# Kernel optimization log

Hardware: AMD Instinct MI355X
Metric: run time of the kernel (lower is better)

The kernel has to match this reference:

```python
import jax, jax.numpy as jnp
import numpy as np

N_NODES = 50000
N_EDGES = 800000
N_FEAT = 128
N_HID = 128
N_LAYER = 4
N_CLASS = 40


def setup_inputs() -> dict:
    key = jax.random.key(0)
    ks = jax.random.split(key, 8)
    x = jax.random.normal(ks[0], (N_NODES, N_FEAT), jnp.float32)
    edge_index = jax.random.randint(ks[1], (2, N_EDGES), 0, N_NODES, dtype=jnp.int64)
    s = 1.0 / np.float32(np.sqrt(N_HID))
    # n_feat == n_hid so all L conv weights stack into one [L, C, C] tensor
    convW = jax.random.normal(ks[2], (N_LAYER, N_HID, N_HID), jnp.float32) * s
    convb = jnp.zeros((N_LAYER, N_HID), jnp.float32)
    W_att = jax.random.normal(ks[3], (N_HID, N_HID), jnp.float32) * s
    a_att = jax.random.normal(ks[4], (N_HID,), jnp.float32) * s
    W_out = jax.random.normal(ks[5], (N_HID, N_CLASS), jnp.float32) * s
    b_out = jnp.zeros((N_CLASS,), jnp.float32)
    return dict(x=x, edge_index=edge_index, convW=convW, convb=convb,
                W_att=W_att, a_att=a_att, W_out=W_out, b_out=b_out)


def reference(x, edge_index, convW, convb, W_att, a_att, W_out, b_out):
    src, dst = edge_index[0], edge_index[1]
    N = x.shape[0]
    # GCN symmetric normalization with self-loops: deg = 1 + in-degree
    deg = jax.ops.segment_sum(jnp.ones_like(dst, dtype=jnp.float32), dst,
                              num_segments=N) + 1.0
    dinv = jax.lax.rsqrt(deg)
    enorm = (dinv[src] * dinv[dst])[:, None]   # per-edge norm
    snorm = (dinv * dinv)[:, None]             # self-loop norm

    hs = []
    h = x
    for l in range(N_LAYER):
        hW = h @ convW[l]                                          # [N, C]
        agg = jax.ops.segment_sum(hW[src] * enorm, dst, num_segments=N)
        agg = agg + hW * snorm                                     # self-loop
        h = jax.nn.relu(agg + convb[l])
        # dropout is identity at inference (training=False)
        hs.append(h)

    H = jnp.stack(hs, axis=1)                                      # [N, L, C]
    # additive attention over layers: alpha_l = softmax_l(a . tanh(W h_l))
    scores = jnp.tanh(H @ W_att) @ a_att                           # [N, L]
    alpha = jax.nn.softmax(scores, axis=1)
    fused = jnp.einsum('nl,nlc->nc', alpha, H)                     # [N, C]
    return fused @ W_out + b_out                                   # [N, n_class]
```

## Files before the change

kernel.cpp:

```cpp
#include <hip/hip_runtime.h>

#define NNODES 50000
#define NEDGES 800000
#define NCLASS 40
#define GEMMB 782
#define XBLK  3125
#define WELL  64

#define EBLK  782
#define PREPB 80
#define WOUTB 6
#define BSHIFT 10
#define NB    49
#define BUCKCAP 20480

typedef _Float16 half8  __attribute__((ext_vector_type(8)));
typedef float    floatx4 __attribute__((ext_vector_type(4)));

#define CSTR 136
#define SMEM_BYTES (64 * CSTR * 2 + 256)

__device__ __forceinline__ float fast_tanh(float x) {
    return 1.0f - 2.0f / (__expf(2.0f * x) + 1.0f);
}

__global__ __launch_bounds__(1024) void k_part(const int* __restrict__ src, const int* __restrict__ dst,
                                               int* __restrict__ gbase, int2* __restrict__ ebuf,
                                               const float* __restrict__ convW, const float* __restrict__ W_att,
                                               _Float16* __restrict__ WT,
                                               const float* __restrict__ Wout, _Float16* __restrict__ WoutT) {
    int bid = blockIdx.x, tid = threadIdx.x;
    if (bid < EBLK) {
        __shared__ int hist[NB];
        __shared__ int base[NB];
        if (tid < NB) hist[tid] = 0;
        __syncthreads();
        int e = bid * 1024 + tid;
        bool ok = e < NEDGES;
        int s = 0, d = 0, b = 0, slot = 0;
        if (ok) {
            d = dst[e];
            s = src[e];
            b = d >> BSHIFT;
            slot = atomicAdd(&hist[b], 1);
        }
        __syncthreads();
        if (tid < NB) base[tid] = atomicAdd(&gbase[tid * 32], hist[tid]);
        __syncthreads();
        if (ok) {
            int pos = base[b] + slot;
            if (pos < BUCKCAP) ebuf[(size_t)b * BUCKCAP + pos] = make_int2(s, d);
        }
    } else if (bid < EBLK + PREPB) {
        int idx = (bid - EBLK) * 1024 + tid;
        int mat = idx >> 14, rem = idx & 16383;
        int j = rem & 7, lane = (rem >> 3) & 63, tile = rem >> 9;
        int l15 = lane & 15, quad = lane >> 4;
        int ct = tile & 7, kk = tile >> 3;
        int n = ct * 16 + l15, k = kk * 32 + quad * 8 + j;
        const float* s = (mat < 4) ? (convW + mat * 16384) : W_att;
        WT[idx] = (_Float16)s[k * 128 + n];
    } else {
        int idx = (bid - EBLK - PREPB) * 1024 + tid;
        int j = idx & 7, lane = (idx >> 3) & 63, tile = idx >> 9;
        int l15 = lane & 15, quad = lane >> 4;
        int ct = tile % 3, kk = tile / 3;
        int n = ct * 16 + l15, k = kk * 32 + quad * 8 + j;
        WoutT[idx] = (n < NCLASS) ? (_Float16)Wout[k * NCLASS + n] : (_Float16)0.f;
    }
}

__global__ __launch_bounds__(1024) void k_build(const int* __restrict__ gbase, const int2* __restrict__ ebuf,
                                                int* __restrict__ esrc, int* __restrict__ cnt) {
    __shared__ int lcnt[1024];
    int b = blockIdx.x, t = threadIdx.x;
    lcnt[t] = 0;
    __syncthreads();
    int n0 = b << BSHIFT;
    int total = gbase[b * 32];
    if (total > BUCKCAP) total = BUCKCAP;
    const int2* ep = ebuf + (size_t)b * BUCKCAP;
    for (int i = t; i < total; i += 1024) {
        int2 p = ep[i];
        int slot = atomicAdd(&lcnt[p.y - n0], 1);
        if (slot < WELL) esrc[p.y * WELL + slot] = p.x;
    }
    __syncthreads();
    int n = n0 + t;
    if (n < NNODES) cnt[n] = (lcnt[t] < WELL) ? lcnt[t] : WELL;
}

__global__ __launch_bounds__(256) void k_gemm0(const float* __restrict__ Av, const _Float16* __restrict__ WTf,
                                               const int* __restrict__ cnt, _Float16* __restrict__ C) {
    __shared__ __align__(16) char smem[SMEM_BYTES];
    _Float16 (*Csh)[CSTR] = (_Float16 (*)[CSTR])smem;
    float* sdinv = (float*)(smem + 64 * CSTR * 2);
    int m0 = blockIdx.x * 64;
    int tid = threadIdx.x;
    int wave = tid >> 6, lane = tid & 63;
    int quad = lane >> 4, l15 = lane & 15;
    int ko = quad * 8;

    if (tid < 64) {
        int r = m0 + tid; if (r > NNODES - 1) r = NNODES - 1;
        sdinv[tid] = rsqrtf((float)cnt[r] + 1.0f);
    }

    floatx4 acc[4][2];
#pragma unroll
    for (int rt = 0; rt < 4; ++rt)
#pragma unroll
        for (int ct = 0; ct < 2; ++ct) acc[rt][ct] = (floatx4){0.f, 0.f, 0.f, 0.f};

#pragma unroll
    for (int kk = 0; kk < 4; ++kk) {
        half8 a[4], b[2];
#pragma unroll
        for (int rt = 0; rt < 4; ++rt) {
            int row = m0 + rt * 16 + l15;
            if (row > NNODES - 1) row = NNODES - 1;
            const float* Ap = Av + (size_t)row * 128 + kk * 32 + ko;
            float4 f0 = *(const float4*)Ap;
            float4 f1 = *(const float4*)(Ap + 4);
            a[rt] = (half8){(_Float16)f0.x, (_Float16)f0.y, (_Float16)f0.z, (_Float16)f0.w,
                            (_Float16)f1.x, (_Float16)f1.y, (_Float16)f1.z, (_Float16)f1.w};
        }
#pragma unroll
        for (int ct = 0; ct < 2; ++ct)
            b[ct] = *(const half8*)&WTf[((kk * 8 + (wave * 2 + ct)) * 64 + lane) * 8];
#pragma unroll
        for (int rt = 0; rt < 4; ++rt)
#pragma unroll
            for (int ct = 0; ct < 2; ++ct)
                acc[rt][ct] = __builtin_amdgcn_mfma_f32_16x16x32_f16(a[rt], b[ct], acc[rt][ct], 0, 0, 0);
    }
    __syncthreads();

#pragma unroll
    for (int rt = 0; rt < 4; ++rt)
#pragma unroll
        for (int r = 0; r < 4; ++r) {
            float d = sdinv[rt * 16 + quad * 4 + r];
#pragma unroll
            for (int ct = 0; ct < 2; ++ct)
                Csh[rt * 16 + quad * 4 + r][wave * 32 + ct * 16 + l15] = (_Float16)(acc[rt][ct][r] * d);
        }
    __syncthreads();

    int row = tid >> 2, seg = tid & 3;
    int gm = m0 + row;
    if (gm < NNODES) {
#pragma unroll
        for (int j = 0; j < 4; ++j)
            *(half8*)(C + (size_t)gm * 128 + seg * 32 + j * 8) = *(const half8*)&Csh[row][seg * 32 + j * 8];
    }
}

template <bool HAS_GEMM>
__global__ __launch_bounds__(128) void k_layer(const _Float16* __restrict__ hin,
                                               const int* __restrict__ cnt, const int* __restrict__ esrc,
                                               const float* __restrict__ bias,
                                               _Float16* __restrict__ hh,
                                               const _Float16* __restrict__ WTatt, const float* __restrict__ a_att,
                                               float* __restrict__ scores, int layer,
                                               const _Float16* __restrict__ WTnext, _Float16* __restrict__ hout) {
    __shared__ __align__(16) _Float16 h[16][CSTR];
    __shared__ float bsh[128];
    __shared__ float sdv[16];
    __shared__ float pp[2][16];
    int tid = threadIdx.x;
    bsh[tid] = bias[tid];
    int wave = tid >> 6, lane = tid & 63;
    int n0 = blockIdx.x * 16;

    {
        int nl = tid >> 3;
        int cl = tid & 7;
        int c16 = cl * 16;
        int n = n0 + nl;
        int cv = cnt[n];
        int beg = n * WELL, end = beg + cv;
        float dn = rsqrtf((float)cv + 1.0f);
        const _Float16* sp = hin + (size_t)n * 128 + c16;
        half8 sv0 = *(const half8*)sp;
        half8 sv1 = *(const half8*)(sp + 8);

        float a[16];
#pragma unroll
        for (int u = 0; u < 16; ++u) a[u] = 0.f;

        int idxA[4]; float mskA[4];
#pragma unroll
        for (int i = 0; i < 4; ++i) {
            int ei = beg + i;
            int t = esrc[ei];
            bool ok = ei < end;
            idxA[i] = ok ? t : n;
            mskA[i] = ok ? 1.f : 0.f;
        }
        for (int e = beg; e < end; e += 4) {
            half8 v0[4], v1[4];
#pragma unroll
            for (int i = 0; i < 4; ++i) {
                const _Float16* p = hin + (size_t)idxA[i] * 128 + c16;
                v0[i] = *(const half8*)p;
                v1[i] = *(const half8*)(p + 8);
            }
            int idxB[4]; float mskB[4];
#pragma unroll
            for (int i = 0; i < 4; ++i) {
                int ei = e + 4 + i;
                int t = esrc[ei];
                bool ok = ei < end;
                idxB[i] = ok ? t : n;
                mskB[i] = ok ? 1.f : 0.f;
            }
#pragma unroll
            for (int i = 0; i < 4; ++i) {
                float m = mskA[i];
#pragma unroll
                for (int u = 0; u < 8; ++u) {
                    a[u]     += m * (float)v0[i][u];
                    a[8 + u] += m * (float)v1[i][u];
                }
            }
#pragma unroll
            for (int i = 0; i < 4; ++i) { idxA[i] = idxB[i]; mskA[i] = mskB[i]; }
        }
        __syncthreads();
        half8 o0, o1;
#pragma unroll
        for (int u = 0; u < 8; ++u) {
            float r0 = (a[u]     + (float)sv0[u]) * dn + bsh[c16 + u];
            float r1 = (a[8 + u] + (float)sv1[u]) * dn + bsh[c16 + 8 + u];
            o0[u] = (_Float16)fmaxf(r0, 0.f);
            o1[u] = (_Float16)fmaxf(r1, 0.f);
        }
        *(half8*)(hh + (size_t)n * 128 + c16)     = o0;
        *(half8*)(hh + (size_t)n * 128 + c16 + 8) = o1;
        *(half8*)&h[nl][c16]     = o0;
        *(half8*)&h[nl][c16 + 8] = o1;
        if (cl == 0) sdv[nl] = dn;
    }
    __syncthreads();

    int quad = lane >> 4, l15 = lane & 15;
    int ko = quad * 8;
    half8 af[4];
#pragma unroll
    for (int kk = 0; kk < 4; ++kk) af[kk] = *(const half8*)&h[l15][kk * 32 + ko];

    {
        float p[4] = {0.f, 0.f, 0.f, 0.f};
#pragma unroll
        for (int c2 = 0; c2 < 4; ++c2) {
            int ct = wave * 4 + c2;
            half8 b[4];
#pragma unroll
            for (int kk = 0; kk < 4; ++kk)
                b[kk] = *(const half8*)&WTatt[((kk * 8 + ct) * 64 + lane) * 8];
            floatx4 acc = (floatx4){0.f, 0.f, 0.f, 0.f};
#pragma unroll
            for (int kk = 0; kk < 4; ++kk)
                acc = __builtin_amdgcn_mfma_f32_16x16x32_f16(af[kk], b[kk], acc, 0, 0, 0);
            float av = a_att[ct * 16 + l15];
#pragma unroll
            for (int r = 0; r < 4; ++r) p[r] += av * fast_tanh(acc[r]);
        }
#pragma unroll
        for (int r = 0; r < 4; ++r) {
            float v = p[r];
            v += __shfl_xor(v, 1); v += __shfl_xor(v, 2);
            v += __shfl_xor(v, 4); v += __shfl_xor(v, 8);
            if (l15 == 0) pp[wave][quad * 4 + r] = v;
        }
    }
    __syncthreads();
    if (tid < 16) scores[(size_t)(n0 + tid) * 4 + layer] = pp[0][tid] + pp[1][tid];

    if (HAS_GEMM) {
        floatx4 acc[4];
#pragma unroll
        for (int c2 = 0; c2 < 4; ++c2) acc[c2] = (floatx4){0.f, 0.f, 0.f, 0.f};
#pragma unroll
        for (int c2 = 0; c2 < 4; ++c2) {
            int ct = wave * 4 + c2;
#pragma unroll
            for (int kk = 0; kk < 4; ++kk) {
                half8 b = *(const half8*)&WTnext[((kk * 8 + ct) * 64 + lane) * 8];
                acc[c2] = __builtin_amdgcn_mfma_f32_16x16x32_f16(af[kk], b, acc[c2], 0, 0, 0);
            }
        }
        __syncthreads();
#pragma unroll
        for (int c2 = 0; c2 < 4; ++c2) {
            int col = wave * 64 + c2 * 16 + l15;
#pragma unroll
            for (int r = 0; r < 4; ++r) {
                int row = quad * 4 + r;
                h[row][col] = (_Float16)(acc[c2][r] * sdv[row]);
            }
        }
        __syncthreads();
        int row = tid >> 3, seg = tid & 7;
        int gm = n0 + row;
        *(half8*)(hout + (size_t)gm * 128 + seg * 16)     = *(const half8*)&h[row][seg * 16];
        *(half8*)(hout + (size_t)gm * 128 + seg * 16 + 8) = *(const half8*)&h[row][seg * 16 + 8];
    }
}

__global__ __launch_bounds__(256) void k_fuse_out(const _Float16* __restrict__ hbase, const float* __restrict__ scores,
                                                  const _Float16* __restrict__ WoutT, const float* __restrict__ bout,
                                                  float* __restrict__ out) {
    __shared__ __align__(16) _Float16 Fs[64][136];
    __shared__ float salpha[256];
    const size_t LSTR = (size_t)NNODES * 128;
    int tid = threadIdx.x;
    int n0 = blockIdx.x * 64;

    if (tid < 64) {
        int node = n0 + tid; if (node > NNODES - 1) node = NNODES - 1;
        float4 s = *(const float4*)(scores + (size_t)node * 4);
        float mx = fmaxf(fmaxf(s.x, s.y), fmaxf(s.z, s.w));
        float e0 = __expf(s.x - mx), e1 = __expf(s.y - mx), e2 = __expf(s.z - mx), e3 = __expf(s.w - mx);
        float inv = 1.0f / (e0 + e1 + e2 + e3);
        salpha[tid * 4 + 0] = e0 * inv; salpha[tid * 4 + 1] = e1 * inv;
        salpha[tid * 4 + 2] = e2 * inv; salpha[tid * 4 + 3] = e3 * inv;
    }
    __syncthreads();

    {
        int no = tid >> 2, seg = tid & 3;
        int node = n0 + no; if (node > NNODES - 1) node = NNODES - 1;
        float al0 = salpha[no * 4 + 0], al1 = salpha[no * 4 + 1];
        float al2 = salpha[no * 4 + 2], al3 = salpha[no * 4 + 3];
        const _Float16* hp = hbase + (size_t)node * 128 + seg * 32;
#pragma unroll
        for (int j = 0; j < 4; ++j) {
            half8 h0 = *(const half8*)(hp + 0 * LSTR + j * 8);
            half8 h1 = *(const half8*)(hp + 1 * LSTR + j * 8);
            half8 h2 = *(const half8*)(hp + 2 * LSTR + j * 8);
            half8 h3 = *(const half8*)(hp + 3 * LSTR + j * 8);
            half8 f;
#pragma unroll
            for (int u = 0; u < 8; ++u)
                f[u] = (_Float16)(al0 * (float)h0[u] + al1 * (float)h1[u] +
                                  al2 * (float)h2[u] + al3 * (float)h3[u]);
            *(half8*)&Fs[no][seg * 32 + j * 8] = f;
        }
    }
    __syncthreads();

    int wave = tid >> 6, lane = tid & 63;
    int quad = lane >> 4, l15 = lane & 15;
    int ko = quad * 8;
    half8 ff[4];
    int frow = wave * 16 + l15;
#pragma unroll
    for (int kk = 0; kk < 4; ++kk) ff[kk] = *(const half8*)&Fs[frow][kk * 32 + ko];
#pragma unroll
    for (int ct = 0; ct < 3; ++ct) {
        half8 bw[4];
#pragma unroll
        for (int kk = 0; kk < 4; ++kk)
            bw[kk] = *(const half8*)(WoutT + ((kk * 3 + ct) * 64 + lane) * 8);
        floatx4 acc = (floatx4){0.f, 0.f, 0.f, 0.f};
#pragma unroll
        for (int kk = 0; kk < 4; ++kk)
            acc = __builtin_amdgcn_mfma_f32_16x16x32_f16(ff[kk], bw[kk], acc, 0, 0, 0);
        int col = ct * 16 + l15;
        if (col < NCLASS) {
            float bv = bout[col];
#pragma unroll
            for (int r = 0; r < 4; ++r) {
                int node = n0 + wave * 16 + quad * 4 + r;
                if (node < NNODES) out[(size_t)node * NCLASS + col] = acc[r] + bv;
            }
        }
    }
}

extern "C" void kernel_launch(void* const* d_in, const int* in_sizes, int n_in,
                              void* d_out, int out_size, void* d_ws, size_t ws_size,
                              hipStream_t stream) {
    const float* x     = (const float*)d_in[0];
    const int*   ei    = (const int*)d_in[1];
    const float* convW = (const float*)d_in[2];
    const float* convb = (const float*)d_in[3];
    const float* W_att = (const float*)d_in[4];
    const float* a_att = (const float*)d_in[5];
    const float* W_out = (const float*)d_in[6];
    const float* b_out = (const float*)d_in[7];
    float* out = (float*)d_out;

    char* ws = (char*)d_ws;
    size_t off = 0;
    auto take = [&](size_t nbytes) { char* p = ws + off; off += (nbytes + 255) & ~(size_t)255; return p; };
    int*       cnt     = (int*)take(NNODES * 4);
    int*       gbase   = (int*)take((size_t)NB * 32 * 4);
    int2*      ebuf    = (int2*)take((size_t)NB * BUCKCAP * 8);
    int*       esrc    = (int*)take((size_t)NNODES * WELL * 4 + 1024);
    _Float16*  WoutT   = (_Float16*)take((size_t)48 * 128 * 2);
    float*     scores  = (float*)take(NNODES * 4 * 4);
    _Float16*  WT      = (_Float16*)take((size_t)5 * 128 * 128 * 2);
    _Float16*  hWsA    = (_Float16*)take((size_t)NNODES * 128 * 2);
    _Float16*  hh[4];
    for (int l = 0; l < 4; ++l) hh[l] = (_Float16*)take((size_t)NNODES * 128 * 2);
    _Float16*  hWsB    = (_Float16*)take((size_t)NNODES * 128 * 2);

    const int* src = ei;
    const int* dst = ei + NEDGES;

    hipMemsetAsync(gbase, 0, (size_t)NB * 32 * 4, stream);
    k_part<<<EBLK + PREPB + WOUTB, 1024, 0, stream>>>(src, dst, gbase, ebuf, convW, W_att, WT, W_out, WoutT);
    k_build<<<NB, 1024, 0, stream>>>(gbase, ebuf, esrc, cnt);
    k_gemm0<<<GEMMB, 256, 0, stream>>>(x, WT, cnt, hWsA);

    k_layer<true><<<XBLK, 128, 0, stream>>>(hWsA, cnt, esrc, convb + 0 * 128, hh[0],
                                            WT + 4 * 16384, a_att, scores, 0, WT + 1 * 16384, hWsB);
    k_layer<true><<<XBLK, 128, 0, stream>>>(hWsB, cnt, esrc, convb + 1 * 128, hh[1],
                                            WT + 4 * 16384, a_att, scores, 1, WT + 2 * 16384, hWsA);
    k_layer<true><<<XBLK, 128, 0, stream>>>(hWsA, cnt, esrc, convb + 2 * 128, hh[2],
                                            WT + 4 * 16384, a_att, scores, 2, WT + 3 * 16384, hWsB);
    k_layer<false><<<XBLK, 128, 0, stream>>>(hWsB, cnt, esrc, convb + 3 * 128, hh[3],
                                             WT + 4 * 16384, a_att, scores, 3, (const _Float16*)nullptr,
                                             (_Float16*)nullptr);
    k_fuse_out<<<GEMMB, 256, 0, stream>>>(hh[0], scores, WoutT, b_out, out);
}
```

Measured before the change: 303.0 us.

## Fuse last GCN layer with attention softmax and output projection; pack edge buffer

The final layer's aggregation, attention score, softmax over layers, weighted fusion and output GEMM now run in one kernel, k_layer_last, so the fourth layer's activations are never written to global memory and the separate fuse kernel launch is gone. The partition buffer also packs (dst offset, src) into a single 32-bit word instead of an int2, halving its traffic. Packing src into 16 bits assumes node indices below 65536. Keeping 16 nodes per block in the output GEMM leaves some waves partly idle.

```diff
diff --git a/kernel.cpp b/kernel.cpp
--- a/kernel.cpp
+++ b/kernel.cpp
@@ -25,7 +25,7 @@
 }
 
 __global__ __launch_bounds__(1024) void k_part(const int* __restrict__ src, const int* __restrict__ dst,
-                                               int* __restrict__ gbase, int2* __restrict__ ebuf,
+                                               int* __restrict__ gbase, unsigned int* __restrict__ ebuf,
                                                const float* __restrict__ convW, const float* __restrict__ W_att,
                                                _Float16* __restrict__ WT,
                                                const float* __restrict__ Wout, _Float16* __restrict__ WoutT) {
@@ -49,7 +49,8 @@
         __syncthreads();
         if (ok) {
             int pos = base[b] + slot;
-            if (pos < BUCKCAP) ebuf[(size_t)b * BUCKCAP + pos] = make_int2(s, d);
+            unsigned int packed = ((unsigned int)(d & ((1 << BSHIFT) - 1)) << 16) | (unsigned int)s;
+            if (pos < BUCKCAP) ebuf[(size_t)b * BUCKCAP + pos] = packed;
         }
     } else if (bid < EBLK + PREPB) {
         int idx = (bid - EBLK) * 1024 + tid;
@@ -70,7 +71,8 @@
     }
 }
 
-__global__ __launch_bounds__(1024) void k_build(const int* __restrict__ gbase, const int2* __restrict__ ebuf,
+__global__ __launch_bounds__(1024) void k_build(const int* __restrict__ gbase,
+                                                const unsigned int* __restrict__ ebuf,
                                                 int* __restrict__ esrc, int* __restrict__ cnt) {
     __shared__ int lcnt[1024];
     int b = blockIdx.x, t = threadIdx.x;
@@ -79,11 +81,13 @@
     int n0 = b << BSHIFT;
     int total = gbase[b * 32];
     if (total > BUCKCAP) total = BUCKCAP;
-    const int2* ep = ebuf + (size_t)b * BUCKCAP;
+    const unsigned int* ep = ebuf + (size_t)b * BUCKCAP;
     for (int i = t; i < total; i += 1024) {
-        int2 p = ep[i];
-        int slot = atomicAdd(&lcnt[p.y - n0], 1);
-        if (slot < WELL) esrc[p.y * WELL + slot] = p.x;
+        unsigned int p = ep[i];
+        int doff = (int)(p >> 16);
+        int s = (int)(p & 0xFFFFu);
+        int slot = atomicAdd(&lcnt[doff], 1);
+        if (slot < WELL) esrc[(n0 + doff) * WELL + slot] = s;
     }
     __syncthreads();
     int n = n0 + t;
@@ -156,7 +160,6 @@
     }
 }
 
-template <bool HAS_GEMM>
 __global__ __launch_bounds__(128) void k_layer(const _Float16* __restrict__ hin,
                                                const int* __restrict__ cnt, const int* __restrict__ esrc,
                                                const float* __restrict__ bias,
@@ -278,7 +281,7 @@
     __syncthreads();
     if (tid < 16) scores[(size_t)(n0 + tid) * 4 + layer] = pp[0][tid] + pp[1][tid];
 
-    if (HAS_GEMM) {
+    {
         floatx4 acc[4];
 #pragma unroll
         for (int c2 = 0; c2 < 4; ++c2) acc[c2] = (floatx4){0.f, 0.f, 0.f, 0.f};
@@ -309,72 +312,181 @@
     }
 }
 
-__global__ __launch_bounds__(256) void k_fuse_out(const _Float16* __restrict__ hbase, const float* __restrict__ scores,
-                                                  const _Float16* __restrict__ WoutT, const float* __restrict__ bout,
-                                                  float* __restrict__ out) {
-    __shared__ __align__(16) _Float16 Fs[64][136];
-    __shared__ float salpha[256];
-    const size_t LSTR = (size_t)NNODES * 128;
+__global__ __launch_bounds__(128) void k_layer_last(const _Float16* __restrict__ hin,
+                                                    const int* __restrict__ cnt, const int* __restrict__ esrc,
+                                                    const float* __restrict__ bias,
+                                                    const _Float16* __restrict__ WTatt,
+                                                    const float* __restrict__ a_att,
+                                                    const float* __restrict__ scores,
+                                                    const _Float16* __restrict__ h0g,
+                                                    const _Float16* __restrict__ h1g,
+                                                    const _Float16* __restrict__ h2g,
+                                                    const _Float16* __restrict__ WoutT,
+                                                    const float* __restrict__ bout,
+                                                    float* __restrict__ out) {
+    __shared__ __align__(16) _Float16 h[16][CSTR];
+    __shared__ float bsh[128];
+    __shared__ float pp[2][16];
     int tid = threadIdx.x;
-    int n0 = blockIdx.x * 64;
-
-    if (tid < 64) {
-        int node = n0 + tid; if (node > NNODES - 1) node = NNODES - 1;
-        float4 s = *(const float4*)(scores + (size_t)node * 4);
-        float mx = fmaxf(fmaxf(s.x, s.y), fmaxf(s.z, s.w));
-        float e0 = __expf(s.x - mx), e1 = __expf(s.y - mx), e2 = __expf(s.z - mx), e3 = __expf(s.w - mx);
-        float inv = 1.0f / (e0 + e1 + e2 + e3);
-        salpha[tid * 4 + 0] = e0 * inv; salpha[tid * 4 + 1] = e1 * inv;
-        salpha[tid * 4 + 2] = e2 * inv; salpha[tid * 4 + 3] = e3 * inv;
-    }
-    __syncthreads();
-
-    {
-        int no = tid >> 2, seg = tid & 3;
-        int node = n0 + no; if (node > NNODES - 1) node = NNODES - 1;
-        float al0 = salpha[no * 4 + 0], al1 = salpha[no * 4 + 1];
-        float al2 = salpha[no * 4 + 2], al3 = salpha[no * 4 + 3];
-        const _Float16* hp = hbase + (size_t)node * 128 + seg * 32;
-#pragma unroll
-        for (int j = 0; j < 4; ++j) {
-            half8 h0 = *(const half8*)(hp + 0 * LSTR + j * 8);
-            half8 h1 = *(const half8*)(hp + 1 * LSTR + j * 8);
-            half8 h2 = *(const half8*)(hp + 2 * LSTR + j * 8);
-            half8 h3 = *(const half8*)(hp + 3 * LSTR + j * 8);
-            half8 f;
-#pragma unroll
-            for (int u = 0; u < 8; ++u)
-                f[u] = (_Float16)(al0 * (float)h0[u] + al1 * (float)h1[u] +
-                                  al2 * (float)h2[u] + al3 * (float)h3[u]);
-            *(half8*)&Fs[no][seg * 32 + j * 8] = f;
-        }
-    }
-    __syncthreads();
-
+    bsh[tid] = bias[tid];
     int wave = tid >> 6, lane = tid & 63;
+    int n0 = blockIdx.x * 16;
+    int nl = tid >> 3, cl = tid & 7, c16 = cl * 16;
+    int n = n0 + nl;
+
+    {
+        int cv = cnt[n];
+        int beg = n * WELL, end = beg + cv;
+        float dn = rsqrtf((float)cv + 1.0f);
+        const _Float16* sp = hin + (size_t)n * 128 + c16;
+        half8 sv0 = *(const half8*)sp;
+        half8 sv1 = *(const half8*)(sp + 8);
+
+        float a[16];
+#pragma unroll
+        for (int u = 0; u < 16; ++u) a[u] = 0.f;
+
+        int idxA[4]; float mskA[4];
+#pragma unroll
+        for (int i = 0; i < 4; ++i) {
+            int ei = beg + i;
+            int t = esrc[ei];
+            bool ok = ei < end;
+            idxA[i] = ok ? t : n;
+            mskA[i] = ok ? 1.f : 0.f;
+        }
+        for (int e = beg; e < end; e += 4) {
+            half8 v0[4], v1[4];
+#pragma unroll
+            for (int i = 0; i < 4; ++i) {
+                const _Float16* p = hin + (size_t)idxA[i] * 128 + c16;
+                v0[i] = *(const half8*)p;
+                v1[i] = *(const half8*)(p + 8);
+            }
+            int idxB[4]; float mskB[4];
+#pragma unroll
+            for (int i = 0; i < 4; ++i) {
+                int ei = e + 4 + i;
+                int t = esrc[ei];
+                bool ok = ei < end;
+                idxB[i] = ok ? t : n;
+                mskB[i] = ok ? 1.f : 0.f;
+            }
+#pragma unroll
+            for (int i = 0; i < 4; ++i) {
+                float m = mskA[i];
+#pragma unroll
+                for (int u = 0; u < 8; ++u) {
+                    a[u]     += m * (float)v0[i][u];
+                    a[8 + u] += m * (float)v1[i][u];
+                }
+            }
+#pragma unroll
+            for (int i = 0; i < 4; ++i) { idxA[i] = idxB[i]; mskA[i] = mskB[i]; }
+        }
+        __syncthreads();
+        half8 o0, o1;
+#pragma unroll
+        for (int u = 0; u < 8; ++u) {
+            float r0 = (a[u]     + (float)sv0[u]) * dn + bsh[c16 + u];
+            float r1 = (a[8 + u] + (float)sv1[u]) * dn + bsh[c16 + 8 + u];
+            o0[u] = (_Float16)fmaxf(r0, 0.f);
+            o1[u] = (_Float16)fmaxf(r1, 0.f);
+        }
+        *(half8*)&h[nl][c16]     = o0;
+        *(half8*)&h[nl][c16 + 8] = o1;
+    }
+    __syncthreads();
+
     int quad = lane >> 4, l15 = lane & 15;
     int ko = quad * 8;
-    half8 ff[4];
-    int frow = wave * 16 + l15;
-#pragma unroll
-    for (int kk = 0; kk < 4; ++kk) ff[kk] = *(const half8*)&Fs[frow][kk * 32 + ko];
-#pragma unroll
-    for (int ct = 0; ct < 3; ++ct) {
-        half8 bw[4];
-#pragma unroll
-        for (int kk = 0; kk < 4; ++kk)
-            bw[kk] = *(const half8*)(WoutT + ((kk * 3 + ct) * 64 + lane) * 8);
-        floatx4 acc = (floatx4){0.f, 0.f, 0.f, 0.f};
-#pragma unroll
-        for (int kk = 0; kk < 4; ++kk)
-            acc = __builtin_amdgcn_mfma_f32_16x16x32_f16(ff[kk], bw[kk], acc, 0, 0, 0);
-        int col = ct * 16 + l15;
-        if (col < NCLASS) {
-            float bv = bout[col];
-#pragma unroll
-            for (int r = 0; r < 4; ++r) {
-                int node = n0 + wave * 16 + quad * 4 + r;
-                if (node < NNODES) out[(size_t)node * NCLASS + col] = acc[r] + bv;
+
+    {
+        half8 af[4];
+#pragma unroll
+        for (int kk = 0; kk < 4; ++kk) af[kk] = *(const half8*)&h[l15][kk * 32 + ko];
+        float p[4] = {0.f, 0.f, 0.f, 0.f};
+#pragma unroll
+        for (int c2 = 0; c2 < 4; ++c2) {
+            int ct = wave * 4 + c2;
+            half8 b[4];
+#pragma unroll
+            for (int kk = 0; kk < 4; ++kk)
+                b[kk] = *(const half8*)&WTatt[((kk * 8 + ct) * 64 + lane) * 8];
+            floatx4 acc = (floatx4){0.f, 0.f, 0.f, 0.f};
+#pragma unroll
+            for (int kk = 0; kk < 4; ++kk)
+                acc = __builtin_amdgcn_mfma_f32_16x16x32_f16(af[kk], b[kk], acc, 0, 0, 0);
+            float av = a_att[ct * 16 + l15];
+#pragma unroll
+            for (int r = 0; r < 4; ++r) p[r] += av * fast_tanh(acc[r]);
+        }
+#pragma unroll
+        for (int r = 0; r < 4; ++r) {
+            float v = p[r];
+            v += __shfl_xor(v, 1); v += __shfl_xor(v, 2);
+            v += __shfl_xor(v, 4); v += __shfl_xor(v, 8);
+            if (l15 == 0) pp[wave][quad * 4 + r] = v;
+        }
+    }
+    __syncthreads();
+
+    {
+        float s0 = scores[(size_t)n * 4 + 0];
+        float s1 = scores[(size_t)n * 4 + 1];
+        float s2 = scores[(size_t)n * 4 + 2];
+        float s3 = pp[0][nl] + pp[1][nl];
+        float mx = fmaxf(fmaxf(s0, s1), fmaxf(s2, s3));
+        float e0 = __expf(s0 - mx), e1 = __expf(s1 - mx), e2 = __expf(s2 - mx), e3 = __expf(s3 - mx);
+        float inv = 1.0f / (e0 + e1 + e2 + e3);
+        float al0 = e0 * inv, al1 = e1 * inv, al2 = e2 * inv, al3 = e3 * inv;
+
+        const _Float16* p0 = h0g + (size_t)n * 128 + c16;
+        const _Float16* p1 = h1g + (size_t)n * 128 + c16;
+        const _Float16* p2 = h2g + (size_t)n * 128 + c16;
+        half8 a0 = *(const half8*)p0, b0 = *(const half8*)(p0 + 8);
+        half8 a1 = *(const half8*)p1, b1 = *(const half8*)(p1 + 8);
+        half8 a2 = *(const half8*)p2, b2 = *(const half8*)(p2 + 8);
+        half8 a3 = *(const half8*)&h[nl][c16], b3 = *(const half8*)&h[nl][c16 + 8];
+        half8 f0, f1;
+#pragma unroll
+        for (int u = 0; u < 8; ++u) {
+            f0[u] = (_Float16)(al0 * (float)a0[u] + al1 * (float)a1[u] +
+                               al2 * (float)a2[u] + al3 * (float)a3[u]);
+            f1[u] = (_Float16)(al0 * (float)b0[u] + al1 * (float)b1[u] +
+                               al2 * (float)b2[u] + al3 * (float)b3[u]);
+        }
+        __syncthreads();
+        *(half8*)&h[nl][c16]     = f0;
+        *(half8*)&h[nl][c16 + 8] = f1;
+    }
+    __syncthreads();
+
+    {
+        half8 ff[4];
+#pragma unroll
+        for (int kk = 0; kk < 4; ++kk) ff[kk] = *(const half8*)&h[l15][kk * 32 + ko];
+        int nct = (wave == 0) ? 2 : 1;
+#pragma unroll
+        for (int c2 = 0; c2 < 2; ++c2) {
+            if (c2 >= nct) break;
+            int ct = (wave == 0) ? c2 : 2;
+            half8 bw[4];
+#pragma unroll
+            for (int kk = 0; kk < 4; ++kk)
+                bw[kk] = *(const half8*)(WoutT + ((kk * 3 + ct) * 64 + lane) * 8);
+            floatx4 acc = (floatx4){0.f, 0.f, 0.f, 0.f};
+#pragma unroll
+            for (int kk = 0; kk < 4; ++kk)
+                acc = __builtin_amdgcn_mfma_f32_16x16x32_f16(ff[kk], bw[kk], acc, 0, 0, 0);
+            int col = ct * 16 + l15;
+            if (col < NCLASS) {
+                float bv = bout[col];
+#pragma unroll
+                for (int r = 0; r < 4; ++r) {
+                    int node = n0 + quad * 4 + r;
+                    out[(size_t)node * NCLASS + col] = acc[r] + bv;
+                }
             }
         }
     }
@@ -396,17 +508,17 @@
     char* ws = (char*)d_ws;
     size_t off = 0;
     auto take = [&](size_t nbytes) { char* p = ws + off; off += (nbytes + 255) & ~(size_t)255; return p; };
-    int*       cnt     = (int*)take(NNODES * 4);
-    int*       gbase   = (int*)take((size_t)NB * 32 * 4);
-    int2*      ebuf    = (int2*)take((size_t)NB * BUCKCAP * 8);
-    int*       esrc    = (int*)take((size_t)NNODES * WELL * 4 + 1024);
-    _Float16*  WoutT   = (_Float16*)take((size_t)48 * 128 * 2);
-    float*     scores  = (float*)take(NNODES * 4 * 4);
-    _Float16*  WT      = (_Float16*)take((size_t)5 * 128 * 128 * 2);
-    _Float16*  hWsA    = (_Float16*)take((size_t)NNODES * 128 * 2);
-    _Float16*  hh[4];
-    for (int l = 0; l < 4; ++l) hh[l] = (_Float16*)take((size_t)NNODES * 128 * 2);
-    _Float16*  hWsB    = (_Float16*)take((size_t)NNODES * 128 * 2);
+    int*          cnt     = (int*)take(NNODES * 4);
+    int*          gbase   = (int*)take((size_t)NB * 32 * 4);
+    unsigned int* ebuf    = (unsigned int*)take((size_t)NB * BUCKCAP * 4);
+    int*          esrc    = (int*)take((size_t)NNODES * WELL * 4 + 1024);
+    _Float16*     WoutT   = (_Float16*)take((size_t)48 * 128 * 2);
+    float*        scores  = (float*)take(NNODES * 4 * 4);
+    _Float16*     WT      = (_Float16*)take((size_t)5 * 128 * 128 * 2);
+    _Float16*     hWsA    = (_Float16*)take((size_t)NNODES * 128 * 2);
+    _Float16*     hh[3];
+    for (int l = 0; l < 3; ++l) hh[l] = (_Float16*)take((size_t)NNODES * 128 * 2);
+    _Float16*     hWsB    = (_Float16*)take((size_t)NNODES * 128 * 2);
 
     const int* src = ei;
     const int* dst = ei + NEDGES;
@@ -416,14 +528,13 @@
     k_build<<<NB, 1024, 0, stream>>>(gbase, ebuf, esrc, cnt);
     k_gemm0<<<GEMMB, 256, 0, stream>>>(x, WT, cnt, hWsA);
 
-    k_layer<true><<<XBLK, 128, 0, stream>>>(hWsA, cnt, esrc, convb + 0 * 128, hh[0],
-                                            WT + 4 * 16384, a_att, scores, 0, WT + 1 * 16384, hWsB);
-    k_layer<true><<<XBLK, 128, 0, stream>>>(hWsB, cnt, esrc, convb + 1 * 128, hh[1],
-                                            WT + 4 * 16384, a_att, scores, 1, WT + 2 * 16384, hWsA);
-    k_layer<true><<<XBLK, 128, 0, stream>>>(hWsA, cnt, esrc, convb + 2 * 128, hh[2],
-                                            WT + 4 * 16384, a_att, scores, 2, WT + 3 * 16384, hWsB);
-    k_layer<false><<<XBLK, 128, 0, stream>>>(hWsB, cnt, esrc, convb + 3 * 128, hh[3],
-                                             WT + 4 * 16384, a_att, scores, 3, (const _Float16*)nullptr,
-                                             (_Float16*)nullptr);
-    k_fuse_out<<<GEMMB, 256, 0, stream>>>(hh[0], scores, WoutT, b_out, out);
-}
+    k_layer<<<XBLK, 128, 0, stream>>>(hWsA, cnt, esrc, convb + 0 * 128, hh[0],
+                                      WT + 4 * 16384, a_att, scores, 0, WT + 1 * 16384, hWsB);
+    k_layer<<<XBLK, 128, 0, stream>>>(hWsB, cnt, esrc, convb + 1 * 128, hh[1],
+                                      WT + 4 * 16384, a_att, scores, 1, WT + 2 * 16384, hWsA);
+    k_layer<<<XBLK, 128, 0, stream>>>(hWsA, cnt, esrc, convb + 2 * 128, hh[2],
+                                      WT + 4 * 16384, a_att, scores, 2, WT + 3 * 16384, hWsB);
+    k_layer_last<<<XBLK, 128, 0, stream>>>(hWsB, cnt, esrc, convb + 3 * 128,
+                                           WT + 4 * 16384, a_att, scores,
+                                           hh[0], hh[1], hh[2], WoutT, b_out, out);
+}
```

New measurement: 286.4 us. 1.06x faster.
